# Performance work log

Measured on AMD Instinct MI355X. Metric: run time of the kernel, lower is better.

## Reference

```python
import jax, jax.numpy as jnp
import numpy as np


def setup_inputs() -> dict:
    key = jax.random.key(0)
    ks = jax.random.split(key, 7)
    b, h, w, c = 4, 64, 64, 256
    fc = 64
    s = 0.05  # small init so exp(-d^2) and softmax stay well-conditioned
    return {
        "feature_map": jax.random.normal(ks[0], (b, h, w, c), dtype=jnp.float32),
        "W_emb": jax.random.normal(ks[1], (fc, c), dtype=jnp.float32) * s,
        "b_emb": jax.random.normal(ks[2], (fc,), dtype=jnp.float32) * s,
        "W_att": jax.random.normal(ks[3], (c, c), dtype=jnp.float32) * s,
        "b_att": jax.random.normal(ks[4], (c,), dtype=jnp.float32) * s,
        "W_thr": jax.random.normal(ks[5], (1, c), dtype=jnp.float32) * s,
        "b_thr": jax.random.normal(ks[6], (1,), dtype=jnp.float32) * s,
        "layer": 0,
    }


def reference(feature_map, W_emb, b_emb, W_att, b_att, W_thr, b_thr, layer):
    # feature_map: (b, h, w, c) channels-last (torch permutes to NCHW; 1x1 convs
    # are pointwise matmuls, so we stay channels-last).
    b, h, w, c = feature_map.shape
    hw = h * w

    # embeddings_conv (1x1): (b,h,w,c) @ (c,fc) -> (b,hw,fc)
    emb = (jnp.einsum('bhwc,fc->bhwf', feature_map, W_emb) + b_emb).reshape(b, hw, -1)

    # ||ei - ej||^2 via expansion (avoids (b,hw,hw,fc) broadcast)
    sq_norm = jnp.sum(emb * emb, axis=-1)  # (b, hw)
    sq_dist = sq_norm[:, :, None] + sq_norm[:, None, :] - 2.0 * jnp.einsum('bif,bjf->bij', emb, emb)
    sq_dist = jnp.maximum(sq_dist, 0.0)
    sim = jnp.exp(-sq_dist)  # (b, hw, hw)

    # attention_conv (1x1)
    shortcut = jnp.einsum('bhwc,dc->bhwd', feature_map, W_att) + b_att  # (b,h,w,c)
    # instance_threshold_conv (1x1) on shortcut -> (b, hw)
    Tinst = (jnp.einsum('bhwc,oc->bhwo', shortcut, W_thr) + b_thr).reshape(b, hw)

    A = jnp.maximum(sim - Tinst[:, None, :], 0.0)
    A = jax.nn.softmax(A, axis=1)  # torch Softmax(dim=1) on (b, hw, hw)

    sc_flat = shortcut.reshape(b, hw, c)  # (b, hw, c)
    # torch: bmm(shortcut(b,c,hw), A^T) -> out[b,c,i] = sum_j sc[b,c,j] * A[b,i,j]
    inst = jnp.einsum('bjc,bij->bic', sc_flat, A).reshape(b, h, w, c)

    return feature_map + inst  # (b, h, w, c)
```

## Files before the change

### kernel.cpp

```cpp
#include <hip/hip_runtime.h>
#include <hip/hip_bf16.h>
#include <math.h>

typedef __attribute__((ext_vector_type(8))) short short8;
typedef __attribute__((ext_vector_type(4))) float f32x4;

#define BB 4
#define HW 4096
#define CC 256
#define FC 64
#define L2E 1.4426950408889634f

#define OFF_EMB   0
#define OFF_SCT2  (2*1024*1024)
#define OFF_SQN   (OFF_SCT2 + 8*1024*1024)
#define OFF_T     (OFF_SQN + 65536)
#define OFF_D     (OFF_T   + 65536)
#define OFF_WEMB2 (OFF_D   + 65536)
#define OFF_WATT2 (OFF_WEMB2 + 32768)

static __device__ __forceinline__ short f2bf(float f) {
    __hip_bfloat16 h = __float2bfloat16(f);
    return *reinterpret_cast<short*>(&h);
}
static __device__ __forceinline__ float bf2f(short s) {
    __hip_bfloat16 h = *reinterpret_cast<__hip_bfloat16*>(&s);
    return __bfloat162float(h);
}
static __device__ __forceinline__ float fexp2(float x) {
#if __has_builtin(__builtin_amdgcn_exp2f)
    return __builtin_amdgcn_exp2f(x);
#else
    float r; asm("v_exp_f32 %0, %1" : "=v"(r) : "v"(x)); return r;
#endif
}
static __device__ __forceinline__ float frcp(float x) {
#if __has_builtin(__builtin_amdgcn_rcpf)
    return __builtin_amdgcn_rcpf(x);
#else
    return 1.0f / x;
#endif
}
#define MFMA32(a, b, c) __builtin_amdgcn_mfma_f32_16x16x32_bf16(a, b, c, 0, 0, 0)

__global__ __launch_bounds__(256) void k_prep(const float* __restrict__ Wemb,
    const float* __restrict__ Watt, short* __restrict__ Wemb2,
    short* __restrict__ Watt2, float* __restrict__ D)
{
    const int bid = blockIdx.x, t = threadIdx.x;
    if (bid < 256) {
        Watt2[(size_t)(t>>3)*2048 + bid*8 + (t&7)] = f2bf(Watt[(size_t)bid*256 + t]);
        if (bid < 64) D[bid*256 + t] = 0.f;
    } else {
        const int f = bid - 256;
        Wemb2[(size_t)(t>>3)*512 + f*8 + (t&7)] = f2bf(Wemb[(size_t)f*256 + t]);
    }
}

__global__ __launch_bounds__(256) void k_front(const float* __restrict__ fm,
    const short* __restrict__ Wemb2, const short* __restrict__ Watt2,
    const float* __restrict__ bemb, const float* __restrict__ batt,
    const float* __restrict__ wthr, const float* __restrict__ bthr,
    short* __restrict__ emb, short* __restrict__ sct2,
    float* __restrict__ sqn, float* __restrict__ T)
{
    const int blk = blockIdx.x;
    const int b = blk >> 8;
    const int r0 = (blk & 255) * 16;
    const int t = threadIdx.x;
    const int w = t >> 6, lane = t & 63, g = lane >> 4, n16 = lane & 15;
    __shared__ short fmt[16*256];
    __shared__ float tred[16][4];
    __shared__ float qred[16][4];
    #pragma unroll
    for (int v = t; v < 512; v += 256) {
        const int row = v >> 5, c32 = v & 31;
        const float4* src = (const float4*)(fm + ((size_t)b*HW + r0 + row)*CC + c32*8);
        float4 x0 = src[0], x1 = src[1];
        short8 pv;
        pv[0]=f2bf(x0.x); pv[1]=f2bf(x0.y); pv[2]=f2bf(x0.z); pv[3]=f2bf(x0.w);
        pv[4]=f2bf(x1.x); pv[5]=f2bf(x1.y); pv[6]=f2bf(x1.z); pv[7]=f2bf(x1.w);
        *(short8*)((char*)fmt + row*512 + ((c32*16) ^ ((row&7)<<4))) = pv;
    }
    __syncthreads();
    const int cb = w*64, fb = w*16;
    f32x4 acc[4], acce;
    #pragma unroll
    for (int nn = 0; nn < 4; ++nn) acc[nn] = (f32x4){0.f,0.f,0.f,0.f};
    acce = (f32x4){0.f,0.f,0.f,0.f};
    #pragma unroll
    for (int kk = 0; kk < 8; ++kk) {
        const int kc = kk*4 + g;
        short8 a = *(const short8*)((const char*)fmt + n16*512 + ((kc*16) ^ ((n16&7)<<4)));
        const short* wb = Watt2 + (size_t)kc*2048 + (cb + n16)*8;
        #pragma unroll
        for (int nn = 0; nn < 4; ++nn) {
            short8 bv = *(const short8*)(wb + nn*128);
            acc[nn] = MFMA32(a, bv, acc[nn]);
        }
        short8 be = *(const short8*)(Wemb2 + (size_t)kc*512 + (fb + n16)*8);
        acce = MFMA32(a, be, acce);
    }
    float tp[4] = {0.f,0.f,0.f,0.f};
    const int jt_ = r0 >> 6;
    const int jc0 = (r0 & 63) >> 3;
    const size_t tilebase = ((size_t)b*64 + jt_)*8;
    #pragma unroll
    for (int nn = 0; nn < 4; ++nn) {
        const int ch = cb + nn*16 + n16;
        const float ba_ = batt[ch], wt_ = wthr[ch];
        float v[4];
        #pragma unroll
        for (int r = 0; r < 4; ++r) { v[r] = acc[nn][r] + ba_; tp[r] = fmaf(v[r], wt_, tp[r]); }
        const int jc = jc0 + (g >> 1);
        const int jw0 = (g & 1)*4;
        short* dstp = sct2 + (tilebase + jc)*2048 + (size_t)ch*8;
        unsigned u01 = (unsigned short)f2bf(v[0]) | ((unsigned)(unsigned short)f2bf(v[1]) << 16);
        unsigned u23 = (unsigned short)f2bf(v[2]) | ((unsigned)(unsigned short)f2bf(v[3]) << 16);
        *(unsigned*)(dstp + jw0)     = u01;
        *(unsigned*)(dstp + jw0 + 2) = u23;
    }
    #pragma unroll
    for (int r = 0; r < 4; ++r)
        #pragma unroll
        for (int off = 1; off <= 8; off <<= 1) tp[r] += __shfl_xor(tp[r], off);
    const int f = fb + n16;
    const float be_ = bemb[f];
    float qp[4];
    #pragma unroll
    for (int r = 0; r < 4; ++r) {
        short bv = f2bf(acce[r] + be_);
        emb[((size_t)b*HW + r0 + g*4 + r)*FC + f] = bv;
        float ef = bf2f(bv);
        qp[r] = ef*ef;
        #pragma unroll
        for (int off = 1; off <= 8; off <<= 1) qp[r] += __shfl_xor(qp[r], off);
    }
    if (n16 == 0) {
        #pragma unroll
        for (int r = 0; r < 4; ++r) { tred[g*4+r][w] = tp[r]; qred[g*4+r][w] = qp[r]; }
    }
    __syncthreads();
    if (t < 16) {
        T[(size_t)b*HW + r0 + t]   = tred[t][0]+tred[t][1]+tred[t][2]+tred[t][3] + bthr[0];
        sqn[(size_t)b*HW + r0 + t] = qred[t][0]+qred[t][1]+qred[t][2]+qred[t][3];
    }
}

__global__ __launch_bounds__(256) void k_colsum(const short* __restrict__ emb,
    const float* __restrict__ sqn, const float* __restrict__ T,
    float* __restrict__ D)
{
    const int bid = blockIdx.x;
    const int split = bid & 7, jt = (bid >> 3) & 63, b = bid >> 9;
    const int t = threadIdx.x, w = t >> 6, lane = t & 63, g = lane >> 4, n16 = lane & 15;
    const size_t jbase = (size_t)b*HW + jt*64;
    __shared__ short ej[64*64];
    __shared__ short ei[2][64*64];
    __shared__ float sqni[2][64];
    #pragma unroll
    for (int v = t; v < 512; v += 256) {
        const int row = v >> 3, c8 = v & 7;
        short8 x = *(const short8*)(emb + (jbase + row)*FC + c8*8);
        *(short8*)((char*)ej + row*128 + ((c8*16) ^ ((row&7)<<4))) = x;
    }
    const int jl = w*16 + n16;
    const float sqjL = -L2E * sqn[jbase + jl];
    const float tjL  = -L2E * T[jbase + jl];
    const int srow0 = t >> 3, srow1 = (t >> 3) + 32, sc8 = t & 7;
    const int sb0 = srow0*128 + ((sc8*16) ^ ((srow0&7)<<4));
    const int sb1 = srow1*128 + ((sc8*16) ^ ((srow1&7)<<4));
    const size_t base0 = (size_t)b*HW + (size_t)split*512;
    short8 stg0 = *(const short8*)(emb + (base0 + srow0)*FC + sc8*8);
    short8 stg1 = *(const short8*)(emb + (base0 + srow1)*FC + sc8*8);
    float stgq = (t < 64) ? sqn[base0 + t] : 0.f;
    *(short8*)((char*)ei[0] + sb0) = stg0;
    *(short8*)((char*)ei[0] + sb1) = stg1;
    if (t < 64) sqni[0][t] = stgq;
    stg0 = *(const short8*)(emb + (base0 + 64 + srow0)*FC + sc8*8);
    stg1 = *(const short8*)(emb + (base0 + 64 + srow1)*FC + sc8*8);
    stgq = (t < 64) ? sqn[base0 + 64 + t] : 0.f;
    __syncthreads();
    const short8 bf0 = *(const short8*)((const char*)ej + jl*128 + ((g*16)     ^ ((jl&7)<<4)));
    const short8 bf1 = *(const short8*)((const char*)ej + jl*128 + (((g+4)*16) ^ ((jl&7)<<4)));
    float csum = 0.f;
    for (int it = 0; it < 8; ++it) {
        if (it < 7) {
            char* eib = (char*)ei[(it+1)&1];
            *(short8*)(eib + sb0) = stg0;
            *(short8*)(eib + sb1) = stg1;
            if (t < 64) sqni[(it+1)&1][t] = stgq;
            if (it < 6) {
                const size_t nb = base0 + (size_t)(it+2)*64;
                stg0 = *(const short8*)(emb + (nb + srow0)*FC + sc8*8);
                stg1 = *(const short8*)(emb + (nb + srow1)*FC + sc8*8);
                stgq = (t < 64) ? sqn[nb + t] : 0.f;
            }
        }
        const char* eib = (const char*)ei[it&1];
        const float* sqc = sqni[it&1];
        #pragma unroll
        for (int m = 0; m < 4; ++m) {
            const int arow = m*16 + n16;
            short8 a0 = *(const short8*)(eib + arow*128 + ((g*16)     ^ ((arow&7)<<4)));
            short8 a1 = *(const short8*)(eib + arow*128 + (((g+4)*16) ^ ((arow&7)<<4)));
            f32x4 dot = {0.f,0.f,0.f,0.f};
            dot = MFMA32(a0, bf0, dot);
            dot = MFMA32(a1, bf1, dot);
            #pragma unroll
            for (int r = 0; r < 4; ++r) {
                float x1 = fminf(fmaf(dot[r], 2.f*L2E, fmaf(-L2E, sqc[m*16 + g*4 + r], sqjL)), 0.f);
                float e1 = fexp2(x1);
                float a_ = fmaxf(fmaf(e1, L2E, tjL), 0.f);
                csum += fexp2(a_);
            }
        }
        __syncthreads();
    }
    csum += __shfl_xor(csum, 16);
    csum += __shfl_xor(csum, 32);
    if (lane < 16) atomicAdd(&D[jbase + jl], csum);
}

#define SCORE_XF(TT, EJB, PW, SQ, TJ, DD)                                      \
  {                                                                            \
    const char* ejb_ = (EJB) + (TT)*8192;                                      \
    short8 b0 = *(const short8*)(ejb_ + jl*128 + ((g*16)     ^ ((jl&7)<<4)));  \
    short8 b1 = *(const short8*)(ejb_ + jl*128 + (((g+4)*16) ^ ((jl&7)<<4)));  \
    const float iD   = frcp(DD);                                               \
    const float sqjL = -L2E * (SQ);                                            \
    const float tjL  = -L2E * (TJ);                                            \
    _Pragma("unroll")                                                          \
    for (int t2 = 0; t2 < 2; ++t2) {                                           \
      f32x4 dot = {0.f,0.f,0.f,0.f};                                           \
      dot = MFMA32(aQ0[t2], b0, dot);                                          \
      dot = MFMA32(aQ1[t2], b1, dot);                                          \
      _Pragma("unroll")                                                        \
      for (int r = 0; r < 4; ++r) {                                            \
        float x1 = fminf(fmaf(dot[r], 2.f*L2E, snL[t2][r] + sqjL), 0.f);       \
        float a_ = fmaxf(fmaf(fexp2(x1), L2E, tjL), 0.f);                      \
        const int prow = ih*32 + t2*16 + g*4 + r;                              \
        *(short*)((PW) + (TT)*8192 + prow*128                                  \
                  + (((jl>>3) ^ (prow&7))<<4) + (jl&7)*2)                      \
            = f2bf(fexp2(a_) * iD);                                            \
      }                                                                        \
    }                                                                          \
  }

#define PV_TILE(TT, PB, BF)                                                    \
  { _Pragma("unroll")                                                          \
    for (int m = 0; m < 4; ++m) {                                              \
      const int prow = m*16 + n16;                                             \
      short8 pa0 = *(const short8*)((PB) + (TT)*8192 + prow*128                \
                                    + (((0*4+g) ^ (prow&7))<<4));              \
      short8 pa1 = *(const short8*)((PB) + (TT)*8192 + prow*128                \
                                    + (((1*4+g) ^ (prow&7))<<4));              \
      _Pragma("unroll")                                                        \
      for (int nn = 0; nn < 2; ++nn) {                                         \
        acc[m][nn] = MFMA32(pa0, (BF)[nn*2+0], acc[m][nn]);                    \
        acc[m][nn] = MFMA32(pa1, (BF)[nn*2+1], acc[m][nn]);                    \
      }                                                                        \
    } }

#define LOAD_BF(DST, TILE)                                                     \
  { const short* sb_ = sct2 + ((size_t)(b*64 + (TILE))*8)*2048                 \
                            + (size_t)(w*32 + n16)*8;                          \
    _Pragma("unroll")                                                          \
    for (int nn = 0; nn < 2; ++nn)                                             \
      _Pragma("unroll")                                                        \
      for (int kc = 0; kc < 2; ++kc)                                           \
        (DST)[nn*2+kc] = *(const short8*)(sb_ + (size_t)(kc*4+g)*2048 + nn*128); }

#define WIN(W, q0C,t0C,d0C, q1C,t1C,d1C, bf0C,bf1C,                            \
            q0N,t0N,d0N, q1N,t1N,d1N, bf0N,bf1N)                               \
  {                                                                            \
    const int k0n = (2*(W)+2 < 64) ? 2*(W)+2 : 63;                             \
    const int k1n = (2*(W)+3 < 64) ? 2*(W)+3 : 63;                             \
    q0N = sqn[bbase + (size_t)k0n*64 + jl];                                    \
    t0N = T  [bbase + (size_t)k0n*64 + jl];                                    \
    d0N = D  [bbase + (size_t)k0n*64 + jl];                                    \
    q1N = sqn[bbase + (size_t)k1n*64 + jl];                                    \
    t1N = T  [bbase + (size_t)k1n*64 + jl];                                    \
    d1N = D  [bbase + (size_t)k1n*64 + jl];                                    \
    LOAD_BF(bf0N, k0n)                                                         \
    LOAD_BF(bf1N, k1n)                                                         \
    const char* Eb = (const char*)ejlds[(W)&1];                                \
    char* Pw = (char*)Plds[(W)&1];                                             \
    SCORE_XF(0, Eb, Pw, q0C, t0C, d0C)                                         \
    SCORE_XF(1, Eb, Pw, q1C, t1C, d1C)                                         \
    { char* En = (char*)ejlds[((W)+1)&1];                                      \
      *(short8*)(En + sbyte) = stgA;                                           \
      *(short8*)(En + 8192 + sbyte) = stgB;                                    \
      const int k0s = (2*(W)+4 < 64) ? 2*(W)+4 : 63;                           \
      const int k1s = (2*(W)+5 < 64) ? 2*(W)+5 : 63;                           \
      stgA = *(const short8*)(emb + (bbase + (size_t)k0s*64 + srow)*FC + sc8*8); \
      stgB = *(const short8*)(emb + (bbase + (size_t)k1s*64 + srow)*FC + sc8*8); \
    }                                                                          \
    __syncthreads();                                                           \
    const char* Pb = (const char*)Plds[(W)&1];                                 \
    __builtin_amdgcn_s_setprio(1);                                             \
    PV_TILE(0, Pb, bf0C)                                                       \
    PV_TILE(1, Pb, bf1C)                                                       \
    __builtin_amdgcn_s_setprio(0);                                             \
  }

__global__ __launch_bounds__(512, 2) void k_attn(const float* __restrict__ fm,
    const short* __restrict__ emb, const float* __restrict__ sqn,
    const float* __restrict__ T, const float* __restrict__ D,
    const short* __restrict__ sct2, float* __restrict__ out)
{
    const int bid = ((blockIdx.x & 7) << 5) | (blockIdx.x >> 3);
    const int b = bid >> 6;
    const int i0 = (bid & 63) * 64;
    const int t = threadIdx.x, w = t >> 6, lane = t & 63, g = lane >> 4, n16 = lane & 15;
    const size_t bbase = (size_t)b * HW;
    const size_t ibase = bbase + i0;
    __shared__ short ejlds[2][2*64*64];
    __shared__ short Plds[2][2*64*64];

    const int ih = w & 1, jq = w >> 1;
    const int jl = jq*16 + n16;

    short8 aQ0[2], aQ1[2];
    float snL[2][4];
    #pragma unroll
    for (int t2 = 0; t2 < 2; ++t2) {
        const size_t qr = ibase + ih*32 + t2*16 + n16;
        aQ0[t2] = *(const short8*)(emb + qr*FC + g*8);
        aQ1[t2] = *(const short8*)(emb + qr*FC + 32 + g*8);
        #pragma unroll
        for (int r = 0; r < 4; ++r)
            snL[t2][r] = -L2E * sqn[ibase + ih*32 + t2*16 + g*4 + r];
    }
    const int srow = t >> 3, sc8 = t & 7;
    const int sbyte = srow*128 + ((sc8*16) ^ ((srow&7)<<4));

    short8 stgA = *(const short8*)(emb + (bbase + srow)*FC + sc8*8);
    short8 stgB = *(const short8*)(emb + (bbase + 64 + srow)*FC + sc8*8);
    *(short8*)((char*)ejlds[0] + sbyte) = stgA;
    *(short8*)((char*)ejlds[0] + 8192 + sbyte) = stgB;
    stgA = *(const short8*)(emb + (bbase + 128 + srow)*FC + sc8*8);
    stgB = *(const short8*)(emb + (bbase + 192 + srow)*FC + sc8*8);
    float q0A = sqn[bbase + jl],      t0A = T[bbase + jl],      d0A = D[bbase + jl];
    float q1A = sqn[bbase + 64 + jl], t1A = T[bbase + 64 + jl], d1A = D[bbase + 64 + jl];
    float q0B, t0B, d0B, q1B, t1B, d1B;
    short8 bf0A[4], bf1A[4], bf0B[4], bf1B[4];
    LOAD_BF(bf0A, 0)
    LOAD_BF(bf1A, 1)
    f32x4 acc[4][2];
    #pragma unroll
    for (int m = 0; m < 4; ++m) {
        acc[m][0] = (f32x4){0.f,0.f,0.f,0.f};
        acc[m][1] = (f32x4){0.f,0.f,0.f,0.f};
    }
    __syncthreads();

    for (int w2 = 0; w2 < 32; w2 += 2) {
        WIN(w2,   q0A,t0A,d0A, q1A,t1A,d1A, bf0A,bf1A,
                  q0B,t0B,d0B, q1B,t1B,d1B, bf0B,bf1B)
        WIN(w2+1, q0B,t0B,d0B, q1B,t1B,d1B, bf0B,bf1B,
                  q0A,t0A,d0A, q1A,t1A,d1A, bf0A,bf1A)
    }

    #pragma unroll
    for (int m = 0; m < 4; ++m)
        #pragma unroll
        for (int r = 0; r < 4; ++r) {
            const size_t row = ibase + m*16 + g*4 + r;
            #pragma unroll
            for (int nn = 0; nn < 2; ++nn) {
                const size_t idx = row*CC + w*32 + nn*16 + n16;
                out[idx] = fm[idx] + acc[m][nn][r];
            }
        }
}

extern "C" void kernel_launch(void* const* d_in, const int* in_sizes, int n_in,
                              void* d_out, int out_size, void* d_ws, size_t ws_size,
                              hipStream_t stream)
{
    const float* fm   = (const float*)d_in[0];
    const float* Wemb = (const float*)d_in[1];
    const float* bemb = (const float*)d_in[2];
    const float* Watt = (const float*)d_in[3];
    const float* batt = (const float*)d_in[4];
    const float* Wthr = (const float*)d_in[5];
    const float* bthr = (const float*)d_in[6];
    char* ws = (char*)d_ws;
    short* emb   = (short*)(ws + OFF_EMB);
    short* sct2  = (short*)(ws + OFF_SCT2);
    float* sqn   = (float*)(ws + OFF_SQN);
    float* T     = (float*)(ws + OFF_T);
    float* D     = (float*)(ws + OFF_D);
    short* Wemb2 = (short*)(ws + OFF_WEMB2);
    short* Watt2 = (short*)(ws + OFF_WATT2);
    float* out = (float*)d_out;

    k_prep  <<<320,  256, 0, stream>>>(Wemb, Watt, Wemb2, Watt2, D);
    k_front <<<1024, 256, 0, stream>>>(fm, Wemb2, Watt2, bemb, batt, Wthr, bthr,
                                       emb, sct2, sqn, T);
    k_colsum<<<2048, 256, 0, stream>>>(emb, sqn, T, D);
    k_attn  <<<256,  512, 0, stream>>>(fm, emb, sqn, T, D, sct2, out);
}
```

Baseline: 106.7 us.

## Materialize exp-scores in bf16 and replace attention recompute with plain GEMM

The column-sum kernel now writes every exp(A) value as bf16 into a large workspace buffer. A separate kernel pre-scales the shortcut values by 1/D, and a new GEMM kernel multiplies the stored scores by the scaled shortcut. This removes the second recomputation of distances and exponentials in the attention kernel. In exchange it adds roughly 128 MB of writes and 128 MB of reads of HBM traffic, and it only runs when the workspace is large enough.

```diff
diff --git a/kernel.cpp b/kernel.cpp
--- a/kernel.cpp
+++ b/kernel.cpp
@@ -3,6 +3,7 @@
 #include <math.h>
 
 typedef __attribute__((ext_vector_type(8))) short short8;
+typedef __attribute__((ext_vector_type(4))) short s16x4;
 typedef __attribute__((ext_vector_type(4))) float f32x4;
 
 #define BB 4
@@ -18,6 +19,9 @@
 #define OFF_D     (OFF_T   + 65536)
 #define OFF_WEMB2 (OFF_D   + 65536)
 #define OFF_WATT2 (OFF_WEMB2 + 32768)
+#define OFF_EXPA  (16*1024*1024)
+#define EXPA_BYTES ((size_t)BB*HW*HW*2)
+#define WS_NEED   ((size_t)OFF_EXPA + EXPA_BYTES)
 
 static __device__ __forceinline__ short f2bf(float f) {
     __hip_bfloat16 h = __float2bfloat16(f);
@@ -144,6 +148,102 @@
     if (t < 16) {
         T[(size_t)b*HW + r0 + t]   = tred[t][0]+tred[t][1]+tred[t][2]+tred[t][3] + bthr[0];
         sqn[(size_t)b*HW + r0 + t] = qred[t][0]+qred[t][1]+qred[t][2]+qred[t][3];
+    }
+}
+
+__global__ __launch_bounds__(256) void k_colsum_w(const short* __restrict__ emb,
+    const float* __restrict__ sqn, const float* __restrict__ T,
+    float* __restrict__ D, short* __restrict__ expA)
+{
+    const int bid = blockIdx.x;
+    const int split = bid & 7, jt = (bid >> 3) & 63, b = bid >> 9;
+    const int t = threadIdx.x, w = t >> 6, lane = t & 63, g = lane >> 4, n16 = lane & 15;
+    const size_t jbase = (size_t)b*HW + jt*64;
+    __shared__ short ej[64*64];
+    __shared__ short ei[2][64*64];
+    __shared__ float sqni[2][64];
+    #pragma unroll
+    for (int v = t; v < 512; v += 256) {
+        const int row = v >> 3, c8 = v & 7;
+        short8 x = *(const short8*)(emb + (jbase + row)*FC + c8*8);
+        *(short8*)((char*)ej + row*128 + ((c8*16) ^ ((row&7)<<4))) = x;
+    }
+    const int jl = w*16 + n16;
+    f32x4 sqjL, tjL;
+    {
+        f32x4 q = *(const f32x4*)(sqn + jbase + w*16 + g*4);
+        f32x4 tt = *(const f32x4*)(T + jbase + w*16 + g*4);
+        #pragma unroll
+        for (int r = 0; r < 4; ++r) { sqjL[r] = -L2E*q[r]; tjL[r] = -L2E*tt[r]; }
+    }
+    const int srow0 = t >> 3, srow1 = (t >> 3) + 32, sc8 = t & 7;
+    const int sb0 = srow0*128 + ((sc8*16) ^ ((srow0&7)<<4));
+    const int sb1 = srow1*128 + ((sc8*16) ^ ((srow1&7)<<4));
+    const size_t base0 = (size_t)b*HW + (size_t)split*512;
+    const int il0 = split*512;
+    short8 stg0 = *(const short8*)(emb + (base0 + srow0)*FC + sc8*8);
+    short8 stg1 = *(const short8*)(emb + (base0 + srow1)*FC + sc8*8);
+    float stgq = (t < 64) ? sqn[base0 + t] : 0.f;
+    *(short8*)((char*)ei[0] + sb0) = stg0;
+    *(short8*)((char*)ei[0] + sb1) = stg1;
+    if (t < 64) sqni[0][t] = stgq;
+    stg0 = *(const short8*)(emb + (base0 + 64 + srow0)*FC + sc8*8);
+    stg1 = *(const short8*)(emb + (base0 + 64 + srow1)*FC + sc8*8);
+    stgq = (t < 64) ? sqn[base0 + 64 + t] : 0.f;
+    __syncthreads();
+    const short8 bf0 = *(const short8*)((const char*)ej + jl*128 + ((g*16)     ^ ((jl&7)<<4)));
+    const short8 bf1 = *(const short8*)((const char*)ej + jl*128 + (((g+4)*16) ^ ((jl&7)<<4)));
+    f32x4 csum = {0.f,0.f,0.f,0.f};
+    short* expAb = expA + (size_t)b*HW*HW;
+    const int jcol = jt*64 + w*16 + g*4;
+    for (int it = 0; it < 8; ++it) {
+        if (it < 7) {
+            char* eib = (char*)ei[(it+1)&1];
+            *(short8*)(eib + sb0) = stg0;
+            *(short8*)(eib + sb1) = stg1;
+            if (t < 64) sqni[(it+1)&1][t] = stgq;
+            if (it < 6) {
+                const size_t nb = base0 + (size_t)(it+2)*64;
+                stg0 = *(const short8*)(emb + (nb + srow0)*FC + sc8*8);
+                stg1 = *(const short8*)(emb + (nb + srow1)*FC + sc8*8);
+                stgq = (t < 64) ? sqn[nb + t] : 0.f;
+            }
+        }
+        const char* eib = (const char*)ei[it&1];
+        const float* sqc = sqni[it&1];
+        #pragma unroll
+        for (int m = 0; m < 4; ++m) {
+            const int arow = m*16 + n16;
+            short8 a0 = *(const short8*)(eib + arow*128 + ((g*16)     ^ ((arow&7)<<4)));
+            short8 a1 = *(const short8*)(eib + arow*128 + (((g+4)*16) ^ ((arow&7)<<4)));
+            f32x4 dot = {0.f,0.f,0.f,0.f};
+            dot = MFMA32(bf0, a0, dot);
+            dot = MFMA32(bf1, a1, dot);
+            const float sniL = -L2E * sqc[m*16 + n16];
+            s16x4 pk;
+            #pragma unroll
+            for (int r = 0; r < 4; ++r) {
+                float x1 = fminf(fmaf(dot[r], 2.f*L2E, sniL + sqjL[r]), 0.f);
+                float a_ = fmaxf(fmaf(fexp2(x1), L2E, tjL[r]), 0.f);
+                float val = fexp2(a_);
+                csum[r] += val;
+                pk[r] = f2bf(val);
+            }
+            const int il = il0 + it*64 + m*16 + n16;
+            *(s16x4*)(expAb + (size_t)il*HW + jcol) = pk;
+        }
+        __syncthreads();
+    }
+    #pragma unroll
+    for (int r = 0; r < 4; ++r) {
+        csum[r] += __shfl_xor(csum[r], 1);
+        csum[r] += __shfl_xor(csum[r], 2);
+        csum[r] += __shfl_xor(csum[r], 4);
+        csum[r] += __shfl_xor(csum[r], 8);
+    }
+    if (n16 == 0) {
+        #pragma unroll
+        for (int r = 0; r < 4; ++r) atomicAdd(&D[jbase + w*16 + g*4 + r], csum[r]);
     }
 }
 
@@ -222,6 +322,85 @@
     if (lane < 16) atomicAdd(&D[jbase + jl], csum);
 }
 
+__global__ __launch_bounds__(256) void k_scale(short* __restrict__ sct2,
+    const float* __restrict__ D)
+{
+    const int v = blockIdx.x*256 + threadIdx.x;
+    const int ch = v & 255, jc = (v >> 8) & 7, jt = (v >> 11) & 63, b = v >> 17;
+    const size_t jb = (size_t)b*HW + jt*64 + jc*8;
+    f32x4 d0 = *(const f32x4*)(D + jb);
+    f32x4 d1 = *(const f32x4*)(D + jb + 4);
+    short8* p = (short8*)(sct2 + ((((size_t)b*64 + jt)*8 + jc)*256 + ch)*8);
+    short8 x = *p;
+    short8 y;
+    y[0] = f2bf(bf2f(x[0]) * frcp(d0[0]));
+    y[1] = f2bf(bf2f(x[1]) * frcp(d0[1]));
+    y[2] = f2bf(bf2f(x[2]) * frcp(d0[2]));
+    y[3] = f2bf(bf2f(x[3]) * frcp(d0[3]));
+    y[4] = f2bf(bf2f(x[4]) * frcp(d1[0]));
+    y[5] = f2bf(bf2f(x[5]) * frcp(d1[1]));
+    y[6] = f2bf(bf2f(x[6]) * frcp(d1[2]));
+    y[7] = f2bf(bf2f(x[7]) * frcp(d1[3]));
+    *p = y;
+}
+
+#define LDA(DST, JT) { _Pragma("unroll") for (int m = 0; m < 2; ++m) {       \
+        const short* p_ = Arow + (size_t)(m*16)*HW + (JT)*64;                \
+        (DST)[m*2+0] = *(const short8*)(p_);                                 \
+        (DST)[m*2+1] = *(const short8*)(p_ + 32); } }
+#define LDB(DST, JT) { const short* q_ = Bbase + (size_t)(JT)*16384;         \
+        _Pragma("unroll") for (int nn = 0; nn < 4; ++nn)                     \
+        _Pragma("unroll") for (int kc = 0; kc < 2; ++kc)                     \
+        (DST)[nn*2+kc] = *(const short8*)(q_ + (kc*4+g)*2048 + nn*128); }
+#define GTILE(AV, BV) { _Pragma("unroll") for (int m = 0; m < 2; ++m)        \
+        _Pragma("unroll") for (int nn = 0; nn < 4; ++nn) {                   \
+        acc[m][nn] = MFMA32((AV)[m*2+0], (BV)[nn*2+0], acc[m][nn]);          \
+        acc[m][nn] = MFMA32((AV)[m*2+1], (BV)[nn*2+1], acc[m][nn]); } }
+
+__global__ __launch_bounds__(256) void k_attn_g(const float* __restrict__ fm,
+    const short* __restrict__ expA, const short* __restrict__ sct2,
+    float* __restrict__ out)
+{
+    const int bid = ((blockIdx.x & 7) << 6) | (blockIdx.x >> 3);
+    const int b = bid >> 7;
+    const int i0 = (bid & 127) * 32;
+    const int t = threadIdx.x, w = t >> 6, lane = t & 63, g = lane >> 4, n16 = lane & 15;
+    const short* Arow  = expA + ((size_t)b*HW + i0 + n16)*HW + g*8;
+    const short* Bbase = sct2 + (size_t)(b*64)*8*2048 + (size_t)(w*64 + n16)*8;
+
+    short8 aA[4], aB[4], bA[8], bB[8];
+    f32x4 acc[2][4];
+    #pragma unroll
+    for (int m = 0; m < 2; ++m)
+        #pragma unroll
+        for (int nn = 0; nn < 4; ++nn) acc[m][nn] = (f32x4){0.f,0.f,0.f,0.f};
+
+    LDA(aA, 0)
+    LDB(bA, 0)
+    for (int jt = 0; jt < 64; jt += 2) {
+        LDA(aB, jt+1)
+        LDB(bB, jt+1)
+        GTILE(aA, bA)
+        const int j2 = (jt+2 < 64) ? jt+2 : 63;
+        LDA(aA, j2)
+        LDB(bA, j2)
+        GTILE(aB, bB)
+    }
+
+    const size_t ibase = (size_t)b*HW + i0;
+    #pragma unroll
+    for (int m = 0; m < 2; ++m)
+        #pragma unroll
+        for (int r = 0; r < 4; ++r) {
+            const size_t row = ibase + m*16 + g*4 + r;
+            #pragma unroll
+            for (int nn = 0; nn < 4; ++nn) {
+                const size_t idx = row*CC + w*64 + nn*16 + n16;
+                out[idx] = fm[idx] + acc[m][nn][r];
+            }
+        }
+}
+
 #define SCORE_XF(TT, EJB, PW, SQ, TJ, DD)                                      \
   {                                                                            \
     const char* ejb_ = (EJB) + (TT)*8192;                                      \
@@ -394,11 +573,18 @@
     float* D     = (float*)(ws + OFF_D);
     short* Wemb2 = (short*)(ws + OFF_WEMB2);
     short* Watt2 = (short*)(ws + OFF_WATT2);
+    short* expA  = (short*)(ws + OFF_EXPA);
     float* out = (float*)d_out;
 
     k_prep  <<<320,  256, 0, stream>>>(Wemb, Watt, Wemb2, Watt2, D);
     k_front <<<1024, 256, 0, stream>>>(fm, Wemb2, Watt2, bemb, batt, Wthr, bthr,
                                        emb, sct2, sqn, T);
-    k_colsum<<<2048, 256, 0, stream>>>(emb, sqn, T, D);
-    k_attn  <<<256,  512, 0, stream>>>(fm, emb, sqn, T, D, sct2, out);
-}
+    if (ws_size >= WS_NEED) {
+        k_colsum_w<<<2048, 256, 0, stream>>>(emb, sqn, T, D, expA);
+        k_scale   <<<2048, 256, 0, stream>>>(sct2, D);
+        k_attn_g  <<<512,  256, 0, stream>>>(fm, expA, sct2, out);
+    } else {
+        k_colsum<<<2048, 256, 0, stream>>>(emb, sqn, T, D);
+        k_attn  <<<256,  512, 0, stream>>>(fm, emb, sqn, T, D, sct2, out);
+    }
+}
```

After: 157.0 us. 1.47x slower.
